# Optimization experiments

Hardware: AMD Instinct MI355X
Metric: run time of the kernel (lower is better)

Reference implementation:

```python
import jax, jax.numpy as jnp
import numpy as np

N, E, G = 20000, 50000, 64          # nodes, edges, graphs
IN_DIM, EDGE_DIM, H, OUT_DIM = 32, 16, 64, 6
EPS = 1e-5  # BatchNorm eps


def setup_inputs() -> dict:
    key = jax.random.key(0)
    ks = jax.random.split(key, 24)
    s = 0.05
    inp = {
        "x": jax.random.normal(ks[0], (N, IN_DIM), jnp.float32),
        "edge_attr": jax.random.normal(ks[1], (E, EDGE_DIM), jnp.float32),
        "src": jax.random.randint(ks[2], (E,), 0, N, jnp.int32),
        "dst": jax.random.randint(ks[3], (E,), 0, N, jnp.int32),
        "batch": jnp.sort(jax.random.randint(ks[4], (N,), 0, G, jnp.int32)),
        # node encoder
        "Wx": jax.random.normal(ks[5], (IN_DIM, H), jnp.float32) * s,
        "bx": jnp.zeros((H,), jnp.float32),
        # three edge MLPs: edge_dim -> H*H
        "We": jax.random.normal(ks[6], (3, EDGE_DIM, H * H), jnp.float32) * s,
        "be": jnp.zeros((3, H * H), jnp.float32),
        # NNConv root weights / biases
        "Wroot": jax.random.normal(ks[7], (3, H, H), jnp.float32) * s,
        "broot": jnp.zeros((3, H), jnp.float32),
        # BatchNorm (eval mode: running stats)
        "gamma": jnp.ones((3, H), jnp.float32),
        "beta": jnp.zeros((3, H), jnp.float32),
        "run_mean": jnp.zeros((3, H), jnp.float32),
        "run_var": jnp.ones((3, H), jnp.float32),
        # head
        "W1": jax.random.normal(ks[8], (H, H), jnp.float32) * s,
        "b1": jnp.zeros((H,), jnp.float32),
        "W2": jax.random.normal(ks[9], (H, OUT_DIM), jnp.float32) * s,
        "b2": jnp.zeros((OUT_DIM,), jnp.float32),
    }
    return inp


def _segment_mean(vals, idx, num_segments):
    tot = jax.ops.segment_sum(vals, idx, num_segments=num_segments)
    cnt = jax.ops.segment_sum(jnp.ones((vals.shape[0],), vals.dtype), idx,
                              num_segments=num_segments)
    return tot / jnp.maximum(cnt, 1.0)[:, None]


def reference(x, edge_attr, src, dst, batch, Wx, bx, We, be, Wroot, broot,
              gamma, beta, run_mean, run_var, W1, b1, W2, b2):
    h = x @ Wx + bx                                      # (N, H)
    for l in range(3):
        # per-edge H x H weight matrices from the edge MLP
        ew = jax.nn.relu(edge_attr @ We[l] + be[l]).reshape(-1, H, H)  # (E, H, H)
        msg = jnp.einsum('eh,eho->eo', h[src], ew)       # gather + per-edge matvec
        agg = _segment_mean(msg, dst, N)                 # scatter-mean at destinations
        out = agg + h @ Wroot[l] + broot[l]              # NNConv root + bias
        out = jax.nn.relu(out)
        # BatchNorm1d in eval mode (running stats); dropout is identity in eval
        out = gamma[l] * (out - run_mean[l]) * jax.lax.rsqrt(run_var[l] + EPS) + beta[l]
        h = out + h                                      # residual (shapes always match)
    pooled = _segment_mean(h, batch, G)                  # global_mean_pool -> (G, H)
    z = jax.nn.relu(pooled @ W1 + b1)
    return z @ W2 + b2                                   # (G, OUT_DIM)
```

## Files before the change

### kernel.cpp

```cpp
#include <hip/hip_runtime.h>
#include <hip/hip_bf16.h>

typedef _Float16 f16x2 __attribute__((ext_vector_type(2)));
typedef _Float16 f16x8 __attribute__((ext_vector_type(8)));
typedef float    f32x4 __attribute__((ext_vector_type(4)));

#define IN_DIM   32
#define EDGE_DIM 16
#define HDIM     64
#define OUT_DIM  6
#define BN_EPS   1e-5f

__global__ void k_prep(const float* __restrict__ ea, _Float16* __restrict__ eaH,
                       const int* __restrict__ dstI, float* __restrict__ deg, int E) {
    int tid = blockIdx.x * 256 + threadIdx.x;
    int E8 = E * 8;
    if (tid < E8) {
        float2 v = ((const float2*)ea)[tid];
        f16x2 r; r[0] = (_Float16)v.x; r[1] = (_Float16)v.y;
        ((f16x2*)eaH)[tid] = r;
    }
    if (tid < E) atomicAdd(&deg[dstI[tid]], 1.0f);
}

__global__ void k_bounds(const int* __restrict__ batch, int* __restrict__ start, int N, int G) {
    int g = threadIdx.x;
    if (g > G) return;
    int lo = 0, hi = N;
    while (lo < hi) { int mid = (lo + hi) >> 1; if (batch[mid] < g) lo = mid + 1; else hi = mid; }
    start[g] = lo;
}

__global__ void k_pack_we(const float* __restrict__ We, uint4* __restrict__ WeB) {
    __shared__ float w[2048];
    int b = blockIdx.x;
    int layer = b >> 5, chunk = b & 31;
    int colbase = chunk * 128;
    int t = threadIdx.x;
    #pragma unroll
    for (int i = 0; i < 8; ++i) {
        int idx = i * 256 + t;
        int k = idx >> 7, c = idx & 127;
        w[idx] = We[(size_t)layer * 65536 + k * 4096 + colbase + c];
    }
    __syncthreads();
    int tile = t >> 5, lane = t & 31;
    int kslot = lane >> 4, col = tile * 16 + (lane & 15);
    f16x8 v;
    #pragma unroll
    for (int j = 0; j < 8; ++j) v[j] = (_Float16)w[(kslot * 8 + j) * 128 + col];
    WeB[(size_t)layer * 8192 + (size_t)(chunk * 8 + tile) * 32 + lane] = __builtin_bit_cast(uint4, v);
}

__global__ void k_encode(const float* __restrict__ x, const float* __restrict__ Wx,
                         const float* __restrict__ bx, float* __restrict__ h, int N) {
    int tid = blockIdx.x * 256 + threadIdx.x;
    int n = tid >> 4, jq = tid & 15;
    if (n >= N) return;
    const float4* W4 = (const float4*)Wx;
    float4 acc = ((const float4*)bx)[jq];
    const float4* xv = (const float4*)(x + (size_t)n * IN_DIM);
    #pragma unroll
    for (int k4 = 0; k4 < 8; ++k4) {
        float4 xk = xv[k4];
        #pragma unroll
        for (int i = 0; i < 4; ++i) {
            float xs = (i == 0) ? xk.x : (i == 1) ? xk.y : (i == 2) ? xk.z : xk.w;
            float4 w = W4[(k4 * 4 + i) * 16 + jq];
            acc.x += xs * w.x; acc.y += xs * w.y; acc.z += xs * w.z; acc.w += xs * w.w;
        }
    }
    ((float4*)h)[tid] = acc;
}

__global__ __launch_bounds__(256, 4) void k_edge(
    const uint4* __restrict__ eaH,
    const uint4* __restrict__ WeB,
    const float* __restrict__ be,
    const float* __restrict__ hin,
    const int* __restrict__ srcI,
    const int* __restrict__ dstI,
    float* __restrict__ agg,
    int E)
{
    __shared__ float hsT[64][68];
    const int t = threadIdx.x;
    const int l = t & 63;
    const int w = t >> 6;
    const int eb = blockIdx.x * 64;

    {
        int el = t >> 2;
        int hq = t & 3;
        int eg = min(eb + el, E - 1);
        int s = srcI[eg];
        const float4* hp = (const float4*)(hin + (size_t)s * HDIM + hq * 16);
        float4 a = hp[0], b = hp[1], c = hp[2], d = hp[3];
        float v[16] = {a.x,a.y,a.z,a.w, b.x,b.y,b.z,b.w, c.x,c.y,c.z,c.w, d.x,d.y,d.z,d.w};
        #pragma unroll
        for (int i = 0; i < 16; ++i) hsT[hq * 16 + i][el] = v[i];
    }
    __syncthreads();

    const int gp  = w >> 1;
    const int oh  = w & 1;
    const int ebw = eb + gp * 32;
    const int elw = gp * 32;
    const int g   = l >> 4;
    const int g4  = g * 4;
    const int c16 = l & 15;

    f16x8 A0 = {}, A1 = {};
    if (g < 2) {
        int e0 = min(ebw + c16, E - 1);
        int e1 = min(ebw + 16 + c16, E - 1);
        A0 = __builtin_bit_cast(f16x8, eaH[(size_t)e0 * 2 + g]);
        A1 = __builtin_bit_cast(f16x8, eaH[(size_t)e1 * 2 + g]);
    }

    f32x4 acc0[2], acc1[2];
    acc0[0] = (f32x4)0.f; acc0[1] = (f32x4)0.f;
    acc1[0] = (f32x4)0.f; acc1[1] = (f32x4)0.f;

    const uint4* Bbase = WeB + (size_t)(l & 31);
    uint4 Bv0 = Bbase[(size_t)(oh * 2 + 0) * 32];
    uint4 Bv1 = Bbase[(size_t)(oh * 2 + 1) * 32];

    for (int h = 0; h < 64; ++h) {
        uint4 Bn0, Bn1;
        if (h < 63) {
            const uint4* Bp = Bbase + (size_t)((h + 1) * 4 + oh * 2) * 32;
            Bn0 = Bp[0]; Bn1 = Bp[32];
        }
        float4 p0 = *(const float4*)&hsT[h][elw + g4];
        float4 p1 = *(const float4*)&hsT[h][elw + 16 + g4];
        float bia0 = be[h * 64 + oh * 32 + c16];
        float bia1 = be[h * 64 + oh * 32 + 16 + c16];

        {
            f16x8 B = __builtin_bit_cast(f16x8, Bv0);
            f32x4 cin = {bia0, bia0, bia0, bia0};
            f32x4 z0 = __builtin_amdgcn_mfma_f32_16x16x32_f16(A0, B, cin, 0, 0, 0);
            f32x4 z1 = __builtin_amdgcn_mfma_f32_16x16x32_f16(A1, B, cin, 0, 0, 0);
            acc0[0][0] += fmaxf(z0[0], 0.f) * p0.x;
            acc0[0][1] += fmaxf(z0[1], 0.f) * p0.y;
            acc0[0][2] += fmaxf(z0[2], 0.f) * p0.z;
            acc0[0][3] += fmaxf(z0[3], 0.f) * p0.w;
            acc1[0][0] += fmaxf(z1[0], 0.f) * p1.x;
            acc1[0][1] += fmaxf(z1[1], 0.f) * p1.y;
            acc1[0][2] += fmaxf(z1[2], 0.f) * p1.z;
            acc1[0][3] += fmaxf(z1[3], 0.f) * p1.w;
        }
        {
            f16x8 B = __builtin_bit_cast(f16x8, Bv1);
            f32x4 cin = {bia1, bia1, bia1, bia1};
            f32x4 z0 = __builtin_amdgcn_mfma_f32_16x16x32_f16(A0, B, cin, 0, 0, 0);
            f32x4 z1 = __builtin_amdgcn_mfma_f32_16x16x32_f16(A1, B, cin, 0, 0, 0);
            acc0[1][0] += fmaxf(z0[0], 0.f) * p0.x;
            acc0[1][1] += fmaxf(z0[1], 0.f) * p0.y;
            acc0[1][2] += fmaxf(z0[2], 0.f) * p0.z;
            acc0[1][3] += fmaxf(z0[3], 0.f) * p0.w;
            acc1[1][0] += fmaxf(z1[0], 0.f) * p1.x;
            acc1[1][1] += fmaxf(z1[1], 0.f) * p1.y;
            acc1[1][2] += fmaxf(z1[2], 0.f) * p1.z;
            acc1[1][3] += fmaxf(z1[3], 0.f) * p1.w;
        }
        Bv0 = Bn0; Bv1 = Bn1;
    }

    #pragma unroll
    for (int grp = 0; grp < 2; ++grp) {
        #pragma unroll
        for (int r = 0; r < 4; ++r) {
            int e = ebw + grp * 16 + g4 + r;
            if (e < E) {
                int d = dstI[e];
                float* base = agg + (size_t)d * HDIM + oh * 32 + c16;
                float v0 = grp == 0 ? acc0[0][r] : acc1[0][r];
                float v1 = grp == 0 ? acc0[1][r] : acc1[1][r];
                atomicAdd(base + 0,  v0);
                atomicAdd(base + 16, v1);
            }
        }
    }
}

__global__ void k_update(
    float* __restrict__ agg, const float* __restrict__ deg,
    const float* __restrict__ hin, const float* __restrict__ Wroot,
    const float* __restrict__ broot, const float* __restrict__ gam,
    const float* __restrict__ bet, const float* __restrict__ rmean,
    const float* __restrict__ rvar, float* __restrict__ hout, int N)
{
    int tid = blockIdx.x * 256 + threadIdx.x;
    int n = tid >> 4, jq = tid & 15;
    if (n >= N) return;
    float dinv = 1.0f / fmaxf(deg[n], 1.0f);
    float4 acc = ((const float4*)broot)[jq];
    float4 ag = ((const float4*)agg)[tid];
    ((float4*)agg)[tid] = make_float4(0.f, 0.f, 0.f, 0.f);
    acc.x += ag.x * dinv; acc.y += ag.y * dinv; acc.z += ag.z * dinv; acc.w += ag.w * dinv;
    const float4* W4 = (const float4*)Wroot;
    const float4* hv = (const float4*)(hin + (size_t)n * HDIM);
    #pragma unroll
    for (int k4 = 0; k4 < 16; ++k4) {
        float4 hk = hv[k4];
        #pragma unroll
        for (int i = 0; i < 4; ++i) {
            float hsc = (i == 0) ? hk.x : (i == 1) ? hk.y : (i == 2) ? hk.z : hk.w;
            float4 w = W4[(k4 * 4 + i) * 16 + jq];
            acc.x += hsc * w.x; acc.y += hsc * w.y; acc.z += hsc * w.z; acc.w += hsc * w.w;
        }
    }
    acc.x = fmaxf(acc.x, 0.f); acc.y = fmaxf(acc.y, 0.f);
    acc.z = fmaxf(acc.z, 0.f); acc.w = fmaxf(acc.w, 0.f);
    float4 g4 = ((const float4*)gam)[jq];
    float4 b4 = ((const float4*)bet)[jq];
    float4 m4 = ((const float4*)rmean)[jq];
    float4 v4 = ((const float4*)rvar)[jq];
    float4 hres = ((const float4*)hin)[tid];
    float4 y;
    y.x = g4.x * (acc.x - m4.x) * rsqrtf(v4.x + BN_EPS) + b4.x + hres.x;
    y.y = g4.y * (acc.y - m4.y) * rsqrtf(v4.y + BN_EPS) + b4.y + hres.y;
    y.z = g4.z * (acc.z - m4.z) * rsqrtf(v4.z + BN_EPS) + b4.z + hres.z;
    y.w = g4.w * (acc.w - m4.w) * rsqrtf(v4.w + BN_EPS) + b4.w + hres.w;
    ((float4*)hout)[tid] = y;
}

__global__ __launch_bounds__(256) void k_pool_head(
    const float* __restrict__ h, const int* __restrict__ start,
    const float* __restrict__ W1, const float* __restrict__ b1,
    const float* __restrict__ W2, const float* __restrict__ b2,
    float* __restrict__ out)
{
    __shared__ float sums[16][68];
    __shared__ float pl[HDIM];
    __shared__ float zl[HDIM];
    int g = blockIdx.x;
    int s0 = start[g], s1 = start[g + 1];
    int t = threadIdx.x, jq = t & 15, rp = t >> 4;
    float4 acc = make_float4(0.f, 0.f, 0.f, 0.f);
    for (int n = s0 + rp; n < s1; n += 16) {
        float4 v = ((const float4*)h)[(size_t)n * 16 + jq];
        acc.x += v.x; acc.y += v.y; acc.z += v.z; acc.w += v.w;
    }
    *(float4*)&sums[rp][jq * 4] = acc;
    __syncthreads();
    if (t < HDIM) {
        float a = 0.f;
        #pragma unroll
        for (int r = 0; r < 16; ++r) a += sums[r][t];
        float cnt = (float)(s1 - s0);
        pl[t] = a / fmaxf(cnt, 1.0f);
    }
    __syncthreads();
    if (t < HDIM) {
        float a = b1[t];
        #pragma unroll
        for (int k = 0; k < HDIM; ++k) a += pl[k] * W1[k * HDIM + t];
        zl[t] = fmaxf(a, 0.f);
    }
    __syncthreads();
    if (t < OUT_DIM) {
        float a = b2[t];
        #pragma unroll
        for (int k = 0; k < HDIM; ++k) a += zl[k] * W2[k * OUT_DIM + t];
        out[(size_t)g * OUT_DIM + t] = a;
    }
}

extern "C" void kernel_launch(void* const* d_in, const int* in_sizes, int n_in,
                              void* d_out, int out_size, void* d_ws, size_t ws_size,
                              hipStream_t stream) {
    const float* x     = (const float*)d_in[0];
    const float* eattr = (const float*)d_in[1];
    const int*   src   = (const int*)d_in[2];
    const int*   dst   = (const int*)d_in[3];
    const int*   batch = (const int*)d_in[4];
    const float* Wx    = (const float*)d_in[5];
    const float* bx    = (const float*)d_in[6];
    const float* We    = (const float*)d_in[7];
    const float* be    = (const float*)d_in[8];
    const float* Wroot = (const float*)d_in[9];
    const float* broot = (const float*)d_in[10];
    const float* gam   = (const float*)d_in[11];
    const float* bet   = (const float*)d_in[12];
    const float* rmean = (const float*)d_in[13];
    const float* rvar  = (const float*)d_in[14];
    const float* W1    = (const float*)d_in[15];
    const float* b1    = (const float*)d_in[16];
    const float* W2    = (const float*)d_in[17];
    const float* b2    = (const float*)d_in[18];
    float* out = (float*)d_out;

    const int N = in_sizes[0] / IN_DIM;
    const int E = in_sizes[2];
    const int G = out_size / OUT_DIM;

    char* ws = (char*)d_ws;
    size_t off = 0;
    auto alloc = [&](size_t bytes) -> void* {
        void* p = ws + off;
        off = (off + bytes + 255) & ~(size_t)255;
        return p;
    };
    float*    h0    = (float*)alloc((size_t)N * HDIM * 4);
    float*    h1    = (float*)alloc((size_t)N * HDIM * 4);
    _Float16* eaH   = (_Float16*)alloc((size_t)E * 16 * 2);
    uint4*    WeB   = (uint4*)alloc((size_t)3 * 8192 * 16);
    int*      start = (int*)alloc((size_t)(G + 1) * 4);
    char*  zbase   = ws + off;
    float* deg     = (float*)alloc((size_t)N * 4);
    float* agg     = (float*)alloc((size_t)N * HDIM * 4);
    size_t zbytes  = (size_t)((ws + off) - zbase);
    (void)ws_size; (void)n_in;

    hipMemsetAsync(zbase, 0, zbytes, stream);

    k_prep<<<(E * 8 + 255) / 256, 256, 0, stream>>>(eattr, eaH, dst, deg, E);
    k_bounds<<<1, 128, 0, stream>>>(batch, start, N, G);
    k_pack_we<<<96, 256, 0, stream>>>(We, WeB);
    k_encode<<<(N * 16 + 255) / 256, 256, 0, stream>>>(x, Wx, bx, h0, N);

    const float* hin = h0;
    float* hout = h1;
    const int edgeBlocks = (E + 63) / 64;
    for (int l = 0; l < 3; ++l) {
        k_edge<<<edgeBlocks, 256, 0, stream>>>(
            (const uint4*)eaH, WeB + (size_t)l * 8192, be + (size_t)l * 4096,
            hin, src, dst, agg, E);
        k_update<<<(N * 16 + 255) / 256, 256, 0, stream>>>(
            agg, deg, hin, Wroot + (size_t)l * 4096, broot + (size_t)l * 64,
            gam + (size_t)l * 64, bet + (size_t)l * 64, rmean + (size_t)l * 64,
            rvar + (size_t)l * 64, hout, N);
        float* tmp = hout; hout = (float*)hin; hin = tmp;
    }
    k_pool_head<<<G, 256, 0, stream>>>(hin, start, W1, b1, W2, b2, out);
}
```

Before: 228.2 us.

## Replace atomic scatter with CSR gather, split edge kernel over input halves

Builds a CSR index of edges by destination (degree count, single-block scan, placement) so k_update gathers per-edge messages instead of k_edge doing float atomics into agg. k_edge is split into two blocks per 64-edge group, each handling half of the input features and writing partial messages to a 2xE buffer, with biases staged in LDS and occupancy hint raised. Setup kernels are fused into one launch and the agg memset is removed. Costs include extra message traffic (2*E*64 floats written and read each layer), a serial single-block scan, and non-deterministic edge order within a row.

```diff
diff --git a/kernel.cpp b/kernel.cpp
--- a/kernel.cpp
+++ b/kernel.cpp
@@ -11,94 +11,149 @@
 #define OUT_DIM  6
 #define BN_EPS   1e-5f
 
-__global__ void k_prep(const float* __restrict__ ea, _Float16* __restrict__ eaH,
-                       const int* __restrict__ dstI, float* __restrict__ deg, int E) {
-    int tid = blockIdx.x * 256 + threadIdx.x;
-    int E8 = E * 8;
-    if (tid < E8) {
-        float2 v = ((const float2*)ea)[tid];
-        f16x2 r; r[0] = (_Float16)v.x; r[1] = (_Float16)v.y;
-        ((f16x2*)eaH)[tid] = r;
-    }
-    if (tid < E) atomicAdd(&deg[dstI[tid]], 1.0f);
-}
-
-__global__ void k_bounds(const int* __restrict__ batch, int* __restrict__ start, int N, int G) {
-    int g = threadIdx.x;
-    if (g > G) return;
-    int lo = 0, hi = N;
-    while (lo < hi) { int mid = (lo + hi) >> 1; if (batch[mid] < g) lo = mid + 1; else hi = mid; }
-    start[g] = lo;
-}
-
-__global__ void k_pack_we(const float* __restrict__ We, uint4* __restrict__ WeB) {
+__global__ __launch_bounds__(256) void k_setup(
+    const float* __restrict__ We, uint4* __restrict__ WeB,
+    const float* __restrict__ x, const float* __restrict__ Wx,
+    const float* __restrict__ bx, float* __restrict__ h,
+    const float* __restrict__ ea, _Float16* __restrict__ eaH,
+    const int* __restrict__ dstI, int* __restrict__ degI,
+    const int* __restrict__ batch, int* __restrict__ start,
+    int N, int E, int G, int PACKB, int ENCB, int PREPB)
+{
     __shared__ float w[2048];
-    int b = blockIdx.x;
-    int layer = b >> 5, chunk = b & 31;
-    int colbase = chunk * 128;
+    int bid = blockIdx.x;
     int t = threadIdx.x;
-    #pragma unroll
-    for (int i = 0; i < 8; ++i) {
-        int idx = i * 256 + t;
-        int k = idx >> 7, c = idx & 127;
-        w[idx] = We[(size_t)layer * 65536 + k * 4096 + colbase + c];
-    }
+
+    if (bid < PACKB) {
+        int layer = bid / 32, chunk = bid % 32;
+        int colbase = chunk * 128;
+        #pragma unroll
+        for (int i = 0; i < 8; ++i) {
+            int idx = i * 256 + t;
+            int k = idx >> 7, c = idx & 127;
+            w[idx] = We[(size_t)layer * 65536 + k * 4096 + colbase + c];
+        }
+        __syncthreads();
+        int tile = t >> 5, lane = t & 31;
+        int kslot = lane >> 4, col = tile * 16 + (lane & 15);
+        f16x8 v;
+        #pragma unroll
+        for (int j = 0; j < 8; ++j) v[j] = (_Float16)w[(kslot * 8 + j) * 128 + col];
+        WeB[(size_t)layer * 8192 + (size_t)(chunk * 8 + tile) * 32 + lane] = __builtin_bit_cast(uint4, v);
+        return;
+    }
+    bid -= PACKB;
+    if (bid < ENCB) {
+        int tid = bid * 256 + t;
+        int n = tid >> 4, jq = tid & 15;
+        if (n >= N) return;
+        const float4* W4 = (const float4*)Wx;
+        float4 acc = ((const float4*)bx)[jq];
+        const float4* xv = (const float4*)(x + (size_t)n * IN_DIM);
+        #pragma unroll
+        for (int k4 = 0; k4 < 8; ++k4) {
+            float4 xk = xv[k4];
+            #pragma unroll
+            for (int i = 0; i < 4; ++i) {
+                float xs = (i == 0) ? xk.x : (i == 1) ? xk.y : (i == 2) ? xk.z : xk.w;
+                float4 ww = W4[(k4 * 4 + i) * 16 + jq];
+                acc.x += xs * ww.x; acc.y += xs * ww.y; acc.z += xs * ww.z; acc.w += xs * ww.w;
+            }
+        }
+        ((float4*)h)[tid] = acc;
+        return;
+    }
+    bid -= ENCB;
+    if (bid < PREPB) {
+        int tid = bid * 256 + t;
+        int E8 = E * 8;
+        if (tid < E8) {
+            float2 v = ((const float2*)ea)[tid];
+            f16x2 r; r[0] = (_Float16)v.x; r[1] = (_Float16)v.y;
+            ((f16x2*)eaH)[tid] = r;
+        }
+        if (tid < E) atomicAdd(&degI[dstI[tid]], 1);
+        return;
+    }
+    if (t <= G) {
+        int lo = 0, hi = N;
+        while (lo < hi) { int mid = (lo + hi) >> 1; if (batch[mid] < t) lo = mid + 1; else hi = mid; }
+        start[t] = lo;
+    }
+}
+
+__global__ void k_scan(const int* __restrict__ degI, int* __restrict__ rowptr,
+                       int* __restrict__ cursor, int N) {
+    __shared__ int buf[256];
+    __shared__ int carry;
+    int t = threadIdx.x;
+    if (t == 0) carry = 0;
     __syncthreads();
-    int tile = t >> 5, lane = t & 31;
-    int kslot = lane >> 4, col = tile * 16 + (lane & 15);
-    f16x8 v;
-    #pragma unroll
-    for (int j = 0; j < 8; ++j) v[j] = (_Float16)w[(kslot * 8 + j) * 128 + col];
-    WeB[(size_t)layer * 8192 + (size_t)(chunk * 8 + tile) * 32 + lane] = __builtin_bit_cast(uint4, v);
-}
-
-__global__ void k_encode(const float* __restrict__ x, const float* __restrict__ Wx,
-                         const float* __restrict__ bx, float* __restrict__ h, int N) {
-    int tid = blockIdx.x * 256 + threadIdx.x;
-    int n = tid >> 4, jq = tid & 15;
-    if (n >= N) return;
-    const float4* W4 = (const float4*)Wx;
-    float4 acc = ((const float4*)bx)[jq];
-    const float4* xv = (const float4*)(x + (size_t)n * IN_DIM);
-    #pragma unroll
-    for (int k4 = 0; k4 < 8; ++k4) {
-        float4 xk = xv[k4];
-        #pragma unroll
-        for (int i = 0; i < 4; ++i) {
-            float xs = (i == 0) ? xk.x : (i == 1) ? xk.y : (i == 2) ? xk.z : xk.w;
-            float4 w = W4[(k4 * 4 + i) * 16 + jq];
-            acc.x += xs * w.x; acc.y += xs * w.y; acc.z += xs * w.z; acc.w += xs * w.w;
-        }
-    }
-    ((float4*)h)[tid] = acc;
-}
-
-__global__ __launch_bounds__(256, 4) void k_edge(
+    for (int base = 0; base < N; base += 256) {
+        int v = (base + t < N) ? degI[base + t] : 0;
+        buf[t] = v;
+        __syncthreads();
+        for (int ofs = 1; ofs < 256; ofs <<= 1) {
+            int xv = (t >= ofs) ? buf[t - ofs] : 0;
+            __syncthreads();
+            buf[t] += xv;
+            __syncthreads();
+        }
+        int excl = buf[t] - v;
+        int total = buf[255];
+        if (base + t < N) {
+            int rp = carry + excl;
+            rowptr[base + t] = rp;
+            cursor[base + t] = rp;
+        }
+        __syncthreads();
+        if (t == 0) carry += total;
+        __syncthreads();
+    }
+    if (t == 0) rowptr[N] = carry;
+}
+
+__global__ void k_place(const int* __restrict__ dstI, int* __restrict__ cursor,
+                        int* __restrict__ eidx, int E) {
+    int e = blockIdx.x * 256 + threadIdx.x;
+    if (e < E) {
+        int p = atomicAdd(&cursor[dstI[e]], 1);
+        eidx[p] = e;
+    }
+}
+
+__global__ __launch_bounds__(256, 6) void k_edge(
     const uint4* __restrict__ eaH,
     const uint4* __restrict__ WeB,
     const float* __restrict__ be,
     const float* __restrict__ hin,
     const int* __restrict__ srcI,
-    const int* __restrict__ dstI,
-    float* __restrict__ agg,
+    float* __restrict__ msgP,
     int E)
 {
-    __shared__ float hsT[64][68];
+    __shared__ float hsT[32][68];
+    __shared__ float beL[2048];
     const int t = threadIdx.x;
     const int l = t & 63;
     const int w = t >> 6;
-    const int eb = blockIdx.x * 64;
+    const int eg = blockIdx.x >> 1;
+    const int hhalf = blockIdx.x & 1;
+    const int eb = eg * 64;
+    const int hbase = hhalf * 32;
 
     {
-        int el = t >> 2;
-        int hq = t & 3;
-        int eg = min(eb + el, E - 1);
-        int s = srcI[eg];
-        const float4* hp = (const float4*)(hin + (size_t)s * HDIM + hq * 16);
-        float4 a = hp[0], b = hp[1], c = hp[2], d = hp[3];
-        float v[16] = {a.x,a.y,a.z,a.w, b.x,b.y,b.z,b.w, c.x,c.y,c.z,c.w, d.x,d.y,d.z,d.w};
-        #pragma unroll
-        for (int i = 0; i < 16; ++i) hsT[hq * 16 + i][el] = v[i];
+        int egc = min(eb + l, E - 1);
+        int s = srcI[egc];
+        const float4* hp = (const float4*)(hin + (size_t)s * HDIM + hbase + w * 8);
+        float4 a = hp[0], b = hp[1];
+        hsT[w*8+0][l] = a.x; hsT[w*8+1][l] = a.y; hsT[w*8+2][l] = a.z; hsT[w*8+3][l] = a.w;
+        hsT[w*8+4][l] = b.x; hsT[w*8+5][l] = b.y; hsT[w*8+6][l] = b.z; hsT[w*8+7][l] = b.w;
+    }
+    {
+        const float4* bg = (const float4*)(be + hbase * 64);
+        float4* bs = (float4*)beL;
+        bs[t] = bg[t];
+        bs[256 + t] = bg[256 + t];
     }
     __syncthreads();
 
@@ -109,6 +164,7 @@
     const int g   = l >> 4;
     const int g4  = g * 4;
     const int c16 = l & 15;
+    const int obase = oh * 32;
 
     f16x8 A0 = {}, A1 = {};
     if (g < 2) {
@@ -118,88 +174,93 @@
         A1 = __builtin_bit_cast(f16x8, eaH[(size_t)e1 * 2 + g]);
     }
 
-    f32x4 acc0[2], acc1[2];
-    acc0[0] = (f32x4)0.f; acc0[1] = (f32x4)0.f;
-    acc1[0] = (f32x4)0.f; acc1[1] = (f32x4)0.f;
+    f32x4 acc00 = (f32x4)0.f, acc01 = (f32x4)0.f;
+    f32x4 acc10 = (f32x4)0.f, acc11 = (f32x4)0.f;
 
     const uint4* Bbase = WeB + (size_t)(l & 31);
-    uint4 Bv0 = Bbase[(size_t)(oh * 2 + 0) * 32];
-    uint4 Bv1 = Bbase[(size_t)(oh * 2 + 1) * 32];
-
-    for (int h = 0; h < 64; ++h) {
+    uint4 Bv0 = Bbase[(size_t)(hbase * 4 + oh * 2 + 0) * 32];
+    uint4 Bv1 = Bbase[(size_t)(hbase * 4 + oh * 2 + 1) * 32];
+
+    for (int hh = 0; hh < 32; ++hh) {
         uint4 Bn0, Bn1;
-        if (h < 63) {
-            const uint4* Bp = Bbase + (size_t)((h + 1) * 4 + oh * 2) * 32;
+        if (hh < 31) {
+            const uint4* Bp = Bbase + (size_t)((hbase + hh + 1) * 4 + oh * 2) * 32;
             Bn0 = Bp[0]; Bn1 = Bp[32];
         }
-        float4 p0 = *(const float4*)&hsT[h][elw + g4];
-        float4 p1 = *(const float4*)&hsT[h][elw + 16 + g4];
-        float bia0 = be[h * 64 + oh * 32 + c16];
-        float bia1 = be[h * 64 + oh * 32 + 16 + c16];
-
+        float4 p0 = *(const float4*)&hsT[hh][elw + g4];
+        float4 p1 = *(const float4*)&hsT[hh][elw + 16 + g4];
+        float bia0 = beL[hh * 64 + obase + c16];
+        float bia1 = beL[hh * 64 + obase + 16 + c16];
         {
             f16x8 B = __builtin_bit_cast(f16x8, Bv0);
             f32x4 cin = {bia0, bia0, bia0, bia0};
             f32x4 z0 = __builtin_amdgcn_mfma_f32_16x16x32_f16(A0, B, cin, 0, 0, 0);
             f32x4 z1 = __builtin_amdgcn_mfma_f32_16x16x32_f16(A1, B, cin, 0, 0, 0);
-            acc0[0][0] += fmaxf(z0[0], 0.f) * p0.x;
-            acc0[0][1] += fmaxf(z0[1], 0.f) * p0.y;
-            acc0[0][2] += fmaxf(z0[2], 0.f) * p0.z;
-            acc0[0][3] += fmaxf(z0[3], 0.f) * p0.w;
-            acc1[0][0] += fmaxf(z1[0], 0.f) * p1.x;
-            acc1[0][1] += fmaxf(z1[1], 0.f) * p1.y;
-            acc1[0][2] += fmaxf(z1[2], 0.f) * p1.z;
-            acc1[0][3] += fmaxf(z1[3], 0.f) * p1.w;
+            acc00[0] += fmaxf(z0[0], 0.f) * p0.x;
+            acc00[1] += fmaxf(z0[1], 0.f) * p0.y;
+            acc00[2] += fmaxf(z0[2], 0.f) * p0.z;
+            acc00[3] += fmaxf(z0[3], 0.f) * p0.w;
+            acc10[0] += fmaxf(z1[0], 0.f) * p1.x;
+            acc10[1] += fmaxf(z1[1], 0.f) * p1.y;
+            acc10[2] += fmaxf(z1[2], 0.f) * p1.z;
+            acc10[3] += fmaxf(z1[3], 0.f) * p1.w;
         }
         {
             f16x8 B = __builtin_bit_cast(f16x8, Bv1);
             f32x4 cin = {bia1, bia1, bia1, bia1};
             f32x4 z0 = __builtin_amdgcn_mfma_f32_16x16x32_f16(A0, B, cin, 0, 0, 0);
             f32x4 z1 = __builtin_amdgcn_mfma_f32_16x16x32_f16(A1, B, cin, 0, 0, 0);
-            acc0[1][0] += fmaxf(z0[0], 0.f) * p0.x;
-            acc0[1][1] += fmaxf(z0[1], 0.f) * p0.y;
-            acc0[1][2] += fmaxf(z0[2], 0.f) * p0.z;
-            acc0[1][3] += fmaxf(z0[3], 0.f) * p0.w;
-            acc1[1][0] += fmaxf(z1[0], 0.f) * p1.x;
-            acc1[1][1] += fmaxf(z1[1], 0.f) * p1.y;
-            acc1[1][2] += fmaxf(z1[2], 0.f) * p1.z;
-            acc1[1][3] += fmaxf(z1[3], 0.f) * p1.w;
+            acc01[0] += fmaxf(z0[0], 0.f) * p0.x;
+            acc01[1] += fmaxf(z0[1], 0.f) * p0.y;
+            acc01[2] += fmaxf(z0[2], 0.f) * p0.z;
+            acc01[3] += fmaxf(z0[3], 0.f) * p0.w;
+            acc11[0] += fmaxf(z1[0], 0.f) * p1.x;
+            acc11[1] += fmaxf(z1[1], 0.f) * p1.y;
+            acc11[2] += fmaxf(z1[2], 0.f) * p1.z;
+            acc11[3] += fmaxf(z1[3], 0.f) * p1.w;
         }
         Bv0 = Bn0; Bv1 = Bn1;
     }
 
+    float* mw = msgP + (size_t)hhalf * E * 64;
     #pragma unroll
     for (int grp = 0; grp < 2; ++grp) {
         #pragma unroll
         for (int r = 0; r < 4; ++r) {
             int e = ebw + grp * 16 + g4 + r;
             if (e < E) {
-                int d = dstI[e];
-                float* base = agg + (size_t)d * HDIM + oh * 32 + c16;
-                float v0 = grp == 0 ? acc0[0][r] : acc1[0][r];
-                float v1 = grp == 0 ? acc0[1][r] : acc1[1][r];
-                atomicAdd(base + 0,  v0);
-                atomicAdd(base + 16, v1);
+                float v0 = grp == 0 ? acc00[r] : acc10[r];
+                float v1 = grp == 0 ? acc01[r] : acc11[r];
+                mw[(size_t)e * 64 + obase + c16]      = v0;
+                mw[(size_t)e * 64 + obase + 16 + c16] = v1;
             }
         }
     }
 }
 
 __global__ void k_update(
-    float* __restrict__ agg, const float* __restrict__ deg,
+    const float* __restrict__ msgP, const int* __restrict__ rowptr,
+    const int* __restrict__ eidx,
     const float* __restrict__ hin, const float* __restrict__ Wroot,
     const float* __restrict__ broot, const float* __restrict__ gam,
     const float* __restrict__ bet, const float* __restrict__ rmean,
-    const float* __restrict__ rvar, float* __restrict__ hout, int N)
+    const float* __restrict__ rvar, float* __restrict__ hout, int N, int E)
 {
     int tid = blockIdx.x * 256 + threadIdx.x;
     int n = tid >> 4, jq = tid & 15;
     if (n >= N) return;
-    float dinv = 1.0f / fmaxf(deg[n], 1.0f);
+    int r0 = rowptr[n], r1 = rowptr[n + 1];
+    float4 s = make_float4(0.f, 0.f, 0.f, 0.f);
+    const float4* m4 = (const float4*)msgP;
+    for (int i = r0; i < r1; ++i) {
+        int eid = eidx[i];
+        float4 a = m4[(size_t)eid * 16 + jq];
+        float4 b = m4[((size_t)E + eid) * 16 + jq];
+        s.x += a.x + b.x; s.y += a.y + b.y; s.z += a.z + b.z; s.w += a.w + b.w;
+    }
+    float dinv = 1.0f / fmaxf((float)(r1 - r0), 1.0f);
     float4 acc = ((const float4*)broot)[jq];
-    float4 ag = ((const float4*)agg)[tid];
-    ((float4*)agg)[tid] = make_float4(0.f, 0.f, 0.f, 0.f);
-    acc.x += ag.x * dinv; acc.y += ag.y * dinv; acc.z += ag.z * dinv; acc.w += ag.w * dinv;
+    acc.x += s.x * dinv; acc.y += s.y * dinv; acc.z += s.z * dinv; acc.w += s.w * dinv;
     const float4* W4 = (const float4*)Wroot;
     const float4* hv = (const float4*)(hin + (size_t)n * HDIM);
     #pragma unroll
@@ -208,22 +269,22 @@
         #pragma unroll
         for (int i = 0; i < 4; ++i) {
             float hsc = (i == 0) ? hk.x : (i == 1) ? hk.y : (i == 2) ? hk.z : hk.w;
-            float4 w = W4[(k4 * 4 + i) * 16 + jq];
-            acc.x += hsc * w.x; acc.y += hsc * w.y; acc.z += hsc * w.z; acc.w += hsc * w.w;
+            float4 ww = W4[(k4 * 4 + i) * 16 + jq];
+            acc.x += hsc * ww.x; acc.y += hsc * ww.y; acc.z += hsc * ww.z; acc.w += hsc * ww.w;
         }
     }
     acc.x = fmaxf(acc.x, 0.f); acc.y = fmaxf(acc.y, 0.f);
     acc.z = fmaxf(acc.z, 0.f); acc.w = fmaxf(acc.w, 0.f);
     float4 g4 = ((const float4*)gam)[jq];
     float4 b4 = ((const float4*)bet)[jq];
-    float4 m4 = ((const float4*)rmean)[jq];
+    float4 mm4 = ((const float4*)rmean)[jq];
     float4 v4 = ((const float4*)rvar)[jq];
     float4 hres = ((const float4*)hin)[tid];
     float4 y;
-    y.x = g4.x * (acc.x - m4.x) * rsqrtf(v4.x + BN_EPS) + b4.x + hres.x;
-    y.y = g4.y * (acc.y - m4.y) * rsqrtf(v4.y + BN_EPS) + b4.y + hres.y;
-    y.z = g4.z * (acc.z - m4.z) * rsqrtf(v4.z + BN_EPS) + b4.z + hres.z;
-    y.w = g4.w * (acc.w - m4.w) * rsqrtf(v4.w + BN_EPS) + b4.w + hres.w;
+    y.x = g4.x * (acc.x - mm4.x) * rsqrtf(v4.x + BN_EPS) + b4.x + hres.x;
+    y.y = g4.y * (acc.y - mm4.y) * rsqrtf(v4.y + BN_EPS) + b4.y + hres.y;
+    y.z = g4.z * (acc.z - mm4.z) * rsqrtf(v4.z + BN_EPS) + b4.z + hres.z;
+    y.w = g4.w * (acc.w - mm4.w) * rsqrtf(v4.w + BN_EPS) + b4.w + hres.w;
     ((float4*)hout)[tid] = y;
 }
 
@@ -304,35 +365,40 @@
         off = (off + bytes + 255) & ~(size_t)255;
         return p;
     };
-    float*    h0    = (float*)alloc((size_t)N * HDIM * 4);
-    float*    h1    = (float*)alloc((size_t)N * HDIM * 4);
-    _Float16* eaH   = (_Float16*)alloc((size_t)E * 16 * 2);
-    uint4*    WeB   = (uint4*)alloc((size_t)3 * 8192 * 16);
-    int*      start = (int*)alloc((size_t)(G + 1) * 4);
-    char*  zbase   = ws + off;
-    float* deg     = (float*)alloc((size_t)N * 4);
-    float* agg     = (float*)alloc((size_t)N * HDIM * 4);
-    size_t zbytes  = (size_t)((ws + off) - zbase);
+    float*    h0     = (float*)alloc((size_t)N * HDIM * 4);
+    float*    h1     = (float*)alloc((size_t)N * HDIM * 4);
+    _Float16* eaH    = (_Float16*)alloc((size_t)E * 16 * 2);
+    uint4*    WeB    = (uint4*)alloc((size_t)3 * 8192 * 16);
+    int*      start  = (int*)alloc((size_t)(G + 1) * 4);
+    int*      rowptr = (int*)alloc((size_t)(N + 1) * 4);
+    int*      cursor = (int*)alloc((size_t)N * 4);
+    int*      eidx   = (int*)alloc((size_t)E * 4);
+    float*    msgP   = (float*)alloc((size_t)2 * E * HDIM * 4);
+    int*      degI   = (int*)alloc((size_t)N * 4);
     (void)ws_size; (void)n_in;
 
-    hipMemsetAsync(zbase, 0, zbytes, stream);
-
-    k_prep<<<(E * 8 + 255) / 256, 256, 0, stream>>>(eattr, eaH, dst, deg, E);
-    k_bounds<<<1, 128, 0, stream>>>(batch, start, N, G);
-    k_pack_we<<<96, 256, 0, stream>>>(We, WeB);
-    k_encode<<<(N * 16 + 255) / 256, 256, 0, stream>>>(x, Wx, bx, h0, N);
+    hipMemsetAsync(degI, 0, (size_t)N * 4, stream);
+
+    const int PACKB = 96;
+    const int ENCB  = (N * 16 + 255) / 256;
+    const int PREPB = (E * 8 + 255) / 256;
+    k_setup<<<PACKB + ENCB + PREPB + 1, 256, 0, stream>>>(
+        We, WeB, x, Wx, bx, h0, eattr, eaH, dst, degI, batch, start,
+        N, E, G, PACKB, ENCB, PREPB);
+    k_scan<<<1, 256, 0, stream>>>(degI, rowptr, cursor, N);
+    k_place<<<(E + 255) / 256, 256, 0, stream>>>(dst, cursor, eidx, E);
 
     const float* hin = h0;
     float* hout = h1;
-    const int edgeBlocks = (E + 63) / 64;
+    const int edgeBlocks = ((E + 63) / 64) * 2;
     for (int l = 0; l < 3; ++l) {
         k_edge<<<edgeBlocks, 256, 0, stream>>>(
             (const uint4*)eaH, WeB + (size_t)l * 8192, be + (size_t)l * 4096,
-            hin, src, dst, agg, E);
+            hin, src, msgP, E);
         k_update<<<(N * 16 + 255) / 256, 256, 0, stream>>>(
-            agg, deg, hin, Wroot + (size_t)l * 4096, broot + (size_t)l * 64,
+            msgP, rowptr, eidx, hin, Wroot + (size_t)l * 4096, broot + (size_t)l * 64,
             gam + (size_t)l * 64, bet + (size_t)l * 64, rmean + (size_t)l * 64,
-            rvar + (size_t)l * 64, hout, N);
+            rvar + (size_t)l * 64, hout, N, E);
         float* tmp = hout; hout = (float*)hin; hin = tmp;
     }
     k_pool_head<<<G, 256, 0, stream>>>(hin, start, W1, b1, W2, b2, out);
```

Result: slower. 271.8 us (+19.1%).
